# Optimization experiments

Hardware: AMD Instinct MI355X
Metric: run time of the kernel (lower is better)

## Reference

```python
import jax, jax.numpy as jnp
import numpy as np

TEMPERATURE = 0.1


def setup_inputs() -> dict:
    key = jax.random.key(0)
    k1, k2 = jax.random.split(key)
    B, D = 8192, 128
    predicted = jax.random.normal(k1, (B, D), dtype=jnp.float32)
    target = jax.random.normal(k2, (B, D), dtype=jnp.float32)
    return {"predicted": predicted, "target": target}


def reference(predicted, target):
    p = predicted.astype(jnp.float32)
    t = target.astype(jnp.float32)
    # Pairwise squared L2 distances via the Gram identity:
    # ||p_i - t_j||^2 = ||p_i||^2 + ||t_j||^2 - 2 p_i . t_j
    # Avoids the O(B*B*D) expanded intermediate of the torch original.
    p_sq = jnp.sum(p * p, axis=1)  # [B]
    t_sq = jnp.sum(t * t, axis=1)  # [B]
    sq = p_sq[:, None] + t_sq[None, :] - 2.0 * jnp.einsum('id,jd->ij', p, t)  # [B, B]
    distances = jnp.sqrt(jnp.maximum(sq, 0.0))
    logits = -distances / TEMPERATURE  # [B, B]
    # Cross-entropy with labels = arange(B): mean over rows of (logsumexp - diag)
    lse = jax.nn.logsumexp(logits, axis=1)  # [B]
    correct = jnp.diagonal(logits)          # [B]
    loss = jnp.mean(lse - correct)
    return loss
```

## Files before the change

### kernel.cpp

```cpp
#include <hip/hip_runtime.h>
#include <hip/hip_bf16.h>


#define NB 8192
#define ND 128

typedef unsigned short u16;
typedef unsigned int u32;

constexpr float TEMP_INV = 10.0f;
constexpr float LN2 = 0.6931471805599453f;
constexpr float C2 = 14.426950408889634f;
constexpr float SHIFT = 180.0f;

typedef __attribute__((ext_vector_type(8))) short short8;
typedef __attribute__((ext_vector_type(16))) float f32x16;

#if __has_builtin(__builtin_amdgcn_exp2f)
#define EXP2(x) __builtin_amdgcn_exp2f(x)
#else
#define EXP2(x) exp2f(x)
#endif
#if __has_builtin(__builtin_amdgcn_logf)
#define LOG2(x) __builtin_amdgcn_logf(x)
#else
#define LOG2(x) log2f(x)
#endif
#if __has_builtin(__builtin_amdgcn_sqrtf)
#define SQRTF(x) __builtin_amdgcn_sqrtf(x)
#else
#define SQRTF(x) sqrtf(x)
#endif

__device__ inline u32 f32_to_bf16_rtne(float x) {
    u32 u = __float_as_uint(x);
    return (u + 0x7FFFu + ((u >> 16) & 1u)) >> 16;
}

__device__ inline void stage16(const u16* __restrict__ g, u16* l) {
    __builtin_amdgcn_global_load_lds(
        (const __attribute__((address_space(1))) void*)g,
        (__attribute__((address_space(3))) void*)l,
        16, 0, 0);
}

__global__ __launch_bounds__(256) void prep_kernel(
    const float* __restrict__ p, const float* __restrict__ t,
    u16* __restrict__ p_t, u16* __restrict__ t_t,
    float* __restrict__ p_sq, float* __restrict__ t_sq,
    float* __restrict__ diag)
{
    int wid  = blockIdx.x * 4 + (threadIdx.x >> 6);
    int lane = threadIdx.x & 63;
    bool is_t = wid >= NB;
    int row = is_t ? wid - NB : wid;
    const float* src = is_t ? t : p;

    float2 v = *(const float2*)(src + (size_t)row * ND + lane * 2);
    u32 packed = f32_to_bf16_rtne(v.x) | (f32_to_bf16_rtne(v.y) << 16);

    int tile = row >> 5, r = row & 31;
    int ks = lane >> 3, hi2 = (lane >> 2) & 1, c4 = lane & 3;
    u32* dstw = (u32*)(is_t ? t_t : p_t) +
                ((size_t)tile * 2048 + ks * 256 + hi2 * 128 + r * 4 + c4);
    *dstw = packed;

    float sq  = v.x * v.x + v.y * v.y;
    float dsq = 0.0f;
    if (is_t) {
        float2 pv = *(const float2*)(p + (size_t)row * ND + lane * 2);
        float d0 = pv.x - v.x, d1 = pv.y - v.y;
        dsq = d0 * d0 + d1 * d1;
    }
    #pragma unroll
    for (int m = 1; m < 64; m <<= 1) {
        sq  += __shfl_xor(sq,  m, 64);
        dsq += __shfl_xor(dsq, m, 64);
    }
    if (lane == 0) {
        if (is_t) { t_sq[row] = sq; diag[row] = -TEMP_INV * SQRTF(dsq); }
        else      { p_sq[row] = sq; }
    }
}

__global__ __launch_bounds__(512, 4) void fused_kernel(
    const u16* __restrict__ p_t, const u16* __restrict__ t_t,
    const float* __restrict__ p_sq, const float* __restrict__ t_sq,
    float* __restrict__ partial)
{
    __shared__ __align__(16) u16 bt[2][4096];
    int tid  = threadIdx.x;
    int w    = tid >> 6;
    int lane = tid & 63;
    int l31  = lane & 31;
    int hi   = lane >> 5;
    int rb   = blockIdx.x & 31;
    int cc   = blockIdx.x >> 5;
    int row_base = rb * 256 + w * 32;
    int tile_a   = rb * 8 + w;
    int jt0      = cc * 8;

    short8 a[8];
    const u16* abase = p_t + (size_t)tile_a * 4096 + lane * 8;
    #pragma unroll
    for (int ks = 0; ks < 8; ++ks)
        a[ks] = *(const short8*)(abase + ks * 512);

    float psq_h[16];
    #pragma unroll
    for (int v = 0; v < 16; ++v)
        psq_h[v] = -0.5f * p_sq[row_base + (v & 3) + 8 * (v >> 2) + 4 * hi];

    float s[16];
    #pragma unroll
    for (int v = 0; v < 16; ++v) s[v] = 0.0f;

    stage16(t_t + (size_t)jt0 * 4096 + tid * 8, &bt[0][tid * 8]);
    __syncthreads();

    for (int it = 0; it < 8; ++it) {
        int buf = it & 1;
        if (it < 7)
            stage16(t_t + (size_t)(jt0 + it + 1) * 4096 + tid * 8,
                    &bt[buf ^ 1][tid * 8]);

        float tsq = t_sq[(jt0 + it) * 32 + l31];

        short8 b[8];
        #pragma unroll
        for (int ks = 0; ks < 8; ++ks)
            b[ks] = *(const short8*)&bt[buf][ks * 512 + lane * 8];

        f32x16 acc;
        #pragma unroll
        for (int v = 0; v < 16; ++v)
            acc[v] = fmaf(tsq, -0.5f, psq_h[v]);

        #pragma unroll
        for (int ks = 0; ks < 8; ++ks)
            acc = __builtin_amdgcn_mfma_f32_32x32x16_bf16(a[ks], b[ks], acc, 0, 0, 0);

        #pragma unroll
        for (int v = 0; v < 16; ++v) {
            float sq = fmaxf(acc[v] * -2.0f, 0.0f);
            float dd = SQRTF(sq);
            float e  = fmaf(dd, -C2, SHIFT);
            s[v] += EXP2(e);
        }

        if (it < 7) __syncthreads();
    }

    #pragma unroll
    for (int v = 0; v < 16; ++v) {
        float x = s[v];
        #pragma unroll
        for (int m = 1; m < 32; m <<= 1) x += __shfl_xor(x, m, 64);
        s[v] = x;
    }
    if (l31 == 0) {
        float* dst = partial + (size_t)cc * NB + row_base;
        #pragma unroll
        for (int v = 0; v < 16; ++v)
            dst[(v & 3) + 8 * (v >> 2) + 4 * hi] = s[v];
    }
}

__global__ __launch_bounds__(256) void reduce1_kernel(
    const float* __restrict__ partial, const float* __restrict__ diag,
    float* __restrict__ block_part)
{
    __shared__ float acc[4];
    int r = blockIdx.x * 256 + threadIdx.x;
    float tot = 0.0f;
    #pragma unroll
    for (int c = 0; c < 32; ++c) tot += partial[(size_t)c * NB + r];
    float lse = LN2 * (LOG2(tot) - SHIFT);
    float lsum = lse - diag[r];
    #pragma unroll
    for (int m = 1; m < 64; m <<= 1) lsum += __shfl_xor(lsum, m, 64);
    if ((threadIdx.x & 63) == 0) acc[threadIdx.x >> 6] = lsum;
    __syncthreads();
    if (threadIdx.x == 0)
        block_part[blockIdx.x] = acc[0] + acc[1] + acc[2] + acc[3];
}

__global__ __launch_bounds__(64) void reduce2_kernel(
    const float* __restrict__ block_part, float* __restrict__ out)
{
    int l = threadIdx.x;
    float x = (l < 32) ? block_part[l] : 0.0f;
    #pragma unroll
    for (int m = 1; m < 64; m <<= 1) x += __shfl_xor(x, m, 64);
    if (l == 0) out[0] = x / (float)NB;
}

extern "C" void kernel_launch(void* const* d_in, const int* in_sizes, int n_in,
                              void* d_out, int out_size, void* d_ws, size_t ws_size,
                              hipStream_t stream)
{
    const float* p = (const float*)d_in[0];
    const float* t = (const float*)d_in[1];
    char* ws = (char*)d_ws;

    u16*   p_t     = (u16*)ws;
    u16*   t_t     = (u16*)(ws + (size_t)NB * ND * 2);
    float* p_sq    = (float*)(ws + (size_t)NB * ND * 4);
    float* t_sq    = p_sq + NB;
    float* diag    = t_sq + NB;
    float* partial = diag + NB;
    float* block_part = partial + 32 * NB;

    prep_kernel<<<(2 * NB) / 4, 256, 0, stream>>>(p, t, p_t, t_t, p_sq, t_sq, diag);
    fused_kernel<<<1024, 512, 0, stream>>>(p_t, t_t, p_sq, t_sq, partial);
    reduce1_kernel<<<32, 256, 0, stream>>>(partial, diag, block_part);
    reduce2_kernel<<<1, 64, 0, stream>>>(block_part, (float*)d_out);
}
```

Measured before the change: 44.38 us.

## Load B tiles directly from global, fold sign into operands, swizzle blocks

Drops the LDS double-buffered staging of target tiles and their barriers. Each wave now loads its B fragments straight from global memory into registers, relying on L2/cache reuse across the 8 waves. P is stored negated in bf16 and the norm terms are sign-flipped, so the accumulator directly holds half the squared distance. This removes a multiply per element, and the sqrt(2) factor is folded into the exp constant. Block indices are also swizzled to change which column/row tiles run concurrently, aiming for better cache locality. The trade-off is redundant global loads per wave in exchange for no synchronization.

Result: slower. 49.92 us (+12.5%).

```diff
diff --git a/kernel.cpp b/kernel.cpp
--- a/kernel.cpp
+++ b/kernel.cpp
@@ -10,7 +10,7 @@
 
 constexpr float TEMP_INV = 10.0f;
 constexpr float LN2 = 0.6931471805599453f;
-constexpr float C2 = 14.426950408889634f;
+constexpr float C2S = 20.403122292392118f;
 constexpr float SHIFT = 180.0f;
 
 typedef __attribute__((ext_vector_type(8))) short short8;
@@ -37,13 +37,6 @@
     return (u + 0x7FFFu + ((u >> 16) & 1u)) >> 16;
 }
 
-__device__ inline void stage16(const u16* __restrict__ g, u16* l) {
-    __builtin_amdgcn_global_load_lds(
-        (const __attribute__((address_space(1))) void*)g,
-        (__attribute__((address_space(3))) void*)l,
-        16, 0, 0);
-}
-
 __global__ __launch_bounds__(256) void prep_kernel(
     const float* __restrict__ p, const float* __restrict__ t,
     u16* __restrict__ p_t, u16* __restrict__ t_t,
@@ -57,7 +50,9 @@
     const float* src = is_t ? t : p;
 
     float2 v = *(const float2*)(src + (size_t)row * ND + lane * 2);
-    u32 packed = f32_to_bf16_rtne(v.x) | (f32_to_bf16_rtne(v.y) << 16);
+    float sx = is_t ? v.x : -v.x;
+    float sy = is_t ? v.y : -v.y;
+    u32 packed = f32_to_bf16_rtne(sx) | (f32_to_bf16_rtne(sy) << 16);
 
     int tile = row >> 5, r = row & 31;
     int ks = lane >> 3, hi2 = (lane >> 2) & 1, c4 = lane & 3;
@@ -88,14 +83,14 @@
     const float* __restrict__ p_sq, const float* __restrict__ t_sq,
     float* __restrict__ partial)
 {
-    __shared__ __align__(16) u16 bt[2][4096];
     int tid  = threadIdx.x;
     int w    = tid >> 6;
     int lane = tid & 63;
     int l31  = lane & 31;
     int hi   = lane >> 5;
-    int rb   = blockIdx.x & 31;
-    int cc   = blockIdx.x >> 5;
+    int swz  = (blockIdx.x & 7) * 128 + (blockIdx.x >> 3);
+    int cc   = swz >> 5;
+    int rb   = swz & 31;
     int row_base = rb * 256 + w * 32;
     int tile_a   = rb * 8 + w;
     int jt0      = cc * 8;
@@ -109,32 +104,24 @@
     float psq_h[16];
     #pragma unroll
     for (int v = 0; v < 16; ++v)
-        psq_h[v] = -0.5f * p_sq[row_base + (v & 3) + 8 * (v >> 2) + 4 * hi];
+        psq_h[v] = 0.5f * p_sq[row_base + (v & 3) + 8 * (v >> 2) + 4 * hi];
 
     float s[16];
     #pragma unroll
     for (int v = 0; v < 16; ++v) s[v] = 0.0f;
 
-    stage16(t_t + (size_t)jt0 * 4096 + tid * 8, &bt[0][tid * 8]);
-    __syncthreads();
-
     for (int it = 0; it < 8; ++it) {
-        int buf = it & 1;
-        if (it < 7)
-            stage16(t_t + (size_t)(jt0 + it + 1) * 4096 + tid * 8,
-                    &bt[buf ^ 1][tid * 8]);
-
+        const u16* tbase = t_t + (size_t)(jt0 + it) * 4096 + lane * 8;
+        short8 b[8];
+        #pragma unroll
+        for (int ks = 0; ks < 8; ++ks)
+            b[ks] = *(const short8*)(tbase + ks * 512);
         float tsq = t_sq[(jt0 + it) * 32 + l31];
 
-        short8 b[8];
-        #pragma unroll
-        for (int ks = 0; ks < 8; ++ks)
-            b[ks] = *(const short8*)&bt[buf][ks * 512 + lane * 8];
-
         f32x16 acc;
         #pragma unroll
         for (int v = 0; v < 16; ++v)
-            acc[v] = fmaf(tsq, -0.5f, psq_h[v]);
+            acc[v] = fmaf(tsq, 0.5f, psq_h[v]);
 
         #pragma unroll
         for (int ks = 0; ks < 8; ++ks)
@@ -142,13 +129,10 @@
 
         #pragma unroll
         for (int v = 0; v < 16; ++v) {
-            float sq = fmaxf(acc[v] * -2.0f, 0.0f);
-            float dd = SQRTF(sq);
-            float e  = fmaf(dd, -C2, SHIFT);
-            s[v] += EXP2(e);
+            float ac = fmaxf(acc[v], 0.0f);
+            float dd = SQRTF(ac);
+            s[v] += EXP2(fmaf(dd, -C2S, SHIFT));
         }
-
-        if (it < 7) __syncthreads();
     }
 
     #pragma unroll
```

## Overlap MFMA with exp epilogue via double accumulators and fold distance scaling

Applied to the files above, without the earlier changes.

The tile loop is fully unrolled and alternates between two accumulators, so the sqrt/exp2 epilogue of the previous tile can run while the MFMAs for the current tile execute. The prep kernel stores p negated in bf16, so the accumulator directly holds half the squared distance. This removes the per-element multiply by -2, and the sqrt(2) factor is folded into the exp constant. The max(0) clamp is also dropped, and all eight t_sq values are loaded up front. The trade-offs are more live registers under the 512-thread, 4-wave launch bounds, and possible NaNs if bf16 rounding ever makes a squared distance slightly negative.

Result: slower. 94.97 us (+114.0%).

```diff
diff --git a/kernel.cpp b/kernel.cpp
--- a/kernel.cpp
+++ b/kernel.cpp
@@ -10,7 +10,7 @@
 
 constexpr float TEMP_INV = 10.0f;
 constexpr float LN2 = 0.6931471805599453f;
-constexpr float C2 = 14.426950408889634f;
+constexpr float C2S = 20.403122292392118f;
 constexpr float SHIFT = 180.0f;
 
 typedef __attribute__((ext_vector_type(8))) short short8;
@@ -57,7 +57,9 @@
     const float* src = is_t ? t : p;
 
     float2 v = *(const float2*)(src + (size_t)row * ND + lane * 2);
-    u32 packed = f32_to_bf16_rtne(v.x) | (f32_to_bf16_rtne(v.y) << 16);
+    float sx = is_t ? v.x : -v.x;
+    float sy = is_t ? v.y : -v.y;
+    u32 packed = f32_to_bf16_rtne(sx) | (f32_to_bf16_rtne(sy) << 16);
 
     int tile = row >> 5, r = row & 31;
     int ks = lane >> 3, hi2 = (lane >> 2) & 1, c4 = lane & 3;
@@ -109,7 +111,12 @@
     float psq_h[16];
     #pragma unroll
     for (int v = 0; v < 16; ++v)
-        psq_h[v] = -0.5f * p_sq[row_base + (v & 3) + 8 * (v >> 2) + 4 * hi];
+        psq_h[v] = 0.5f * p_sq[row_base + (v & 3) + 8 * (v >> 2) + 4 * hi];
+
+    float tsq[8];
+    #pragma unroll
+    for (int it = 0; it < 8; ++it)
+        tsq[it] = t_sq[(jt0 + it) * 32 + l31];
 
     float s[16];
     #pragma unroll
@@ -118,38 +125,41 @@
     stage16(t_t + (size_t)jt0 * 4096 + tid * 8, &bt[0][tid * 8]);
     __syncthreads();
 
+    f32x16 acc0, acc1;
+
+    #pragma unroll
     for (int it = 0; it < 8; ++it) {
-        int buf = it & 1;
         if (it < 7)
             stage16(t_t + (size_t)(jt0 + it + 1) * 4096 + tid * 8,
-                    &bt[buf ^ 1][tid * 8]);
-
-        float tsq = t_sq[(jt0 + it) * 32 + l31];
+                    &bt[(it & 1) ^ 1][tid * 8]);
 
         short8 b[8];
         #pragma unroll
         for (int ks = 0; ks < 8; ++ks)
-            b[ks] = *(const short8*)&bt[buf][ks * 512 + lane * 8];
-
-        f32x16 acc;
+            b[ks] = *(const short8*)&bt[it & 1][ks * 512 + lane * 8];
+
+        f32x16& acc = (it & 1) ? acc1 : acc0;
         #pragma unroll
         for (int v = 0; v < 16; ++v)
-            acc[v] = fmaf(tsq, -0.5f, psq_h[v]);
+            acc[v] = fmaf(tsq[it], 0.5f, psq_h[v]);
 
         #pragma unroll
         for (int ks = 0; ks < 8; ++ks)
             acc = __builtin_amdgcn_mfma_f32_32x32x16_bf16(a[ks], b[ks], acc, 0, 0, 0);
 
-        #pragma unroll
-        for (int v = 0; v < 16; ++v) {
-            float sq = fmaxf(acc[v] * -2.0f, 0.0f);
-            float dd = SQRTF(sq);
-            float e  = fmaf(dd, -C2, SHIFT);
-            s[v] += EXP2(e);
+        if (it > 0) {
+            f32x16& ap = (it & 1) ? acc0 : acc1;
+            #pragma unroll
+            for (int v = 0; v < 16; ++v)
+                s[v] += EXP2(fmaf(SQRTF(ap[v]), -C2S, SHIFT));
         }
 
         if (it < 7) __syncthreads();
     }
+
+    #pragma unroll
+    for (int v = 0; v < 16; ++v)
+        s[v] += EXP2(fmaf(SQRTF(acc1[v]), -C2S, SHIFT));
 
     #pragma unroll
     for (int v = 0; v < 16; ++v) {
```
